# Kernel tuning notes

Hardware: AMD Instinct MI355X
Metric: run time of the kernel (lower is better)

## Reference

```python
import jax, jax.numpy as jnp
import numpy as np

D_MODEL = 4096
NUM_EXPERTS = 64
TOP_K = 2


def setup_inputs() -> dict:
    key = jax.random.key(0)
    kx, kw, kb = jax.random.split(key, 3)
    x = jax.random.normal(kx, (4, 4096, D_MODEL), dtype=jnp.float32)
    # nn.Linear(d_model, num_experts): weight [E, D], bias [E]
    bound = 1.0 / np.sqrt(D_MODEL)
    W = jax.random.uniform(kw, (NUM_EXPERTS, D_MODEL), jnp.float32, -bound, bound)
    b = jax.random.uniform(kb, (NUM_EXPERTS,), jnp.float32, -bound, bound)
    return {"x": x, "W": W, "b": b}


def reference(x, W, b):
    # gate: logits over experts  [B, S, E]
    logits = jnp.einsum("bsd,ed->bse", x, W) + b
    # top-k experts per token
    top_w, top_i = jax.lax.top_k(logits, TOP_K)  # [B, S, K]
    # softmax over the selected k logits
    top_w = jax.nn.softmax(top_w, axis=-1)
    return top_w, top_i
```

## Files before the change

kernel.cpp:

```cpp
#include <hip/hip_runtime.h>
#include <math.h>

#define D_MODEL 4096
#define NE 64
#define TPB 64
#define NSTEPS 64
#define XBUF 16384
#define NXBUF 4
#define WS_SHORTS (256 * 2 * 64 * 8)

typedef __attribute__((ext_vector_type(8))) short short8;
typedef __attribute__((ext_vector_type(16))) float f32x16;

__device__ __forceinline__ void gl_lds(const void* g, void* l) {
    __builtin_amdgcn_global_load_lds(
        (const __attribute__((address_space(1))) unsigned*)g,
        (__attribute__((address_space(3))) unsigned*)l, 16, 0, 0);
}

__device__ __forceinline__ void split8(const float4& a, const float4& c,
                                       short8& h8, short8& l8) {
    union { short8 s; unsigned u[4]; } H, L;
    float vv[8] = {a.x, a.y, a.z, a.w, c.x, c.y, c.z, c.w};
#pragma unroll
    for (int p = 0; p < 4; p++) {
        const float v0 = vv[2*p], v1 = vv[2*p+1];
        const unsigned u0 = __float_as_uint(v0), u1 = __float_as_uint(v1);
        const unsigned r0 = u0 + 0x7fffu + ((u0 >> 16) & 1u);
        const unsigned r1 = u1 + 0x7fffu + ((u1 >> 16) & 1u);
        const float lo0 = v0 - __uint_as_float(r0 & 0xffff0000u);
        const float lo1 = v1 - __uint_as_float(r1 & 0xffff0000u);
        H.u[p] = __builtin_amdgcn_perm(r1, r0, 0x07060302u);
        L.u[p] = __builtin_amdgcn_perm(__float_as_uint(lo1),
                                       __float_as_uint(lo0), 0x07060302u);
    }
    h8 = H.s; l8 = L.s;
}

__global__ void wsplit_kernel(const float* __restrict__ W, short* __restrict__ wsp) {
    const int ck = blockIdx.x, t = threadIdx.x;
    const int nt = t >> 6, l = t & 63;
    const float* wp = W + (size_t)(nt * 32 + (l & 31)) * D_MODEL + ck * 16 + (l >> 5) * 8;
    float4 a = *(const float4*)wp, c = *(const float4*)(wp + 4);
    union { short8 s; unsigned u[4]; } H, L;
    float vv[8] = {a.x, a.y, a.z, a.w, c.x, c.y, c.z, c.w};
#pragma unroll
    for (int p = 0; p < 4; p++) {
        const float v0 = vv[2*p], v1 = vv[2*p+1];
        const unsigned u0 = __float_as_uint(v0), u1 = __float_as_uint(v1);
        const unsigned r0 = u0 + 0x7fffu + ((u0 >> 16) & 1u);
        const unsigned r1 = u1 + 0x7fffu + ((u1 >> 16) & 1u);
        const float lo0 = v0 - __uint_as_float(r0 & 0xffff0000u);
        const float lo1 = v1 - __uint_as_float(r1 & 0xffff0000u);
        const unsigned q0 = __float_as_uint(lo0) + 0x7fffu + ((__float_as_uint(lo0) >> 16) & 1u);
        const unsigned q1 = __float_as_uint(lo1) + 0x7fffu + ((__float_as_uint(lo1) >> 16) & 1u);
        H.u[p] = __builtin_amdgcn_perm(r1, r0, 0x07060302u);
        L.u[p] = __builtin_amdgcn_perm(q1, q0, 0x07060302u);
    }
    const size_t off = ((size_t)(ck * 2 + nt) * 64 + l) * 8;
    *(short8*)(wsp + off)             = H.s;
    *(short8*)(wsp + WS_SHORTS + off) = L.s;
}

#define MF(A_, B_, n_) acc[n_] = __builtin_amdgcn_mfma_f32_32x32x16_bf16( \
                             A_, B_, acc[n_], 0, 0, 0)

__global__ __launch_bounds__(512, 2) void router_pipe(
    const float* __restrict__ x, const short* __restrict__ wsp,
    const float* __restrict__ b, float* __restrict__ out, int T)
{
    __shared__ char smem[NXBUF * XBUF];

    const int tid  = threadIdx.x;
    const int wv   = tid >> 6, lane = tid & 63;
    const int mt   = wv & 1;
    const int kq   = wv >> 1;
    const int tok0 = blockIdx.x * TPB;

    const int tokA = tid >> 4, clA = tid & 15;
    const int tokB = 32 + tokA;
    const float* gx1 = x + (size_t)(tok0 + tokA) * D_MODEL + ((clA ^ (tokA & 15)) * 4);
    const float* gx2 = x + (size_t)(tok0 + tokB) * D_MODEL + ((clA ^ (tokB & 15)) * 4);

#define STAGEX(s_, bi_) do { char* db_ = smem + (bi_) * XBUF + wv * 1024;      \
        gl_lds(gx1 + (size_t)(s_) * 64, db_);                                  \
        gl_lds(gx2 + (size_t)(s_) * 64, db_ + 8192);                           \
        __builtin_amdgcn_sched_barrier(0); } while (0)

#define LDW(s_, W0_, W1_, W2_, W3_) do {                                       \
        const size_t ck_ = (size_t)(s_) * 4 + kq;                              \
        const size_t o0_ = ((ck_ * 2 + 0) * 64 + lane) * 8;                    \
        const size_t o1_ = ((ck_ * 2 + 1) * 64 + lane) * 8;                    \
        W0_ = *(const short8*)(wsp + o0_);                                     \
        W1_ = *(const short8*)(wsp + o1_);                                     \
        W2_ = *(const short8*)(wsp + WS_SHORTS + o0_);                         \
        W3_ = *(const short8*)(wsp + WS_SHORTS + o1_);                         \
        __builtin_amdgcn_sched_barrier(0); } while (0)

#define FENCE(n_) do { asm volatile("s_waitcnt vmcnt(" #n_ ")" ::: "memory");  \
        __builtin_amdgcn_sched_barrier(0); } while (0)
#define BAR do { __builtin_amdgcn_s_barrier();                                 \
        __builtin_amdgcn_sched_barrier(0); } while (0)

    f32x16 acc[2];
#pragma unroll
    for (int e = 0; e < 16; e++) { acc[0][e] = 0.f; acc[1][e] = 0.f; }

    const int row = mt * 32 + (lane & 31);
    const int c0  = kq * 4 + (lane >> 5) * 2;
    const int xo1 = row * 256 + ((c0       ^ (row & 15)) * 16);
    const int xo2 = row * 256 + (((c0 + 1) ^ (row & 15)) * 16);

#define COMPUTE(bi_, W0_, W1_, W2_, W3_) do {                                  \
        const char* buf_ = smem + (bi_) * XBUF;                                \
        float4 xa_ = *(const float4*)(buf_ + xo1);                             \
        float4 xb_ = *(const float4*)(buf_ + xo2);                             \
        short8 Ah_, Al_;                                                       \
        split8(xa_, xb_, Ah_, Al_);                                            \
        MF(Ah_, W0_, 0); MF(Ah_, W2_, 0); MF(Al_, W0_, 0); MF(Al_, W2_, 0);    \
        MF(Ah_, W1_, 1); MF(Ah_, W3_, 1); MF(Al_, W1_, 1); MF(Al_, W3_, 1); } while (0)

    short8 Wa0, Wa1, Wa2, Wa3, Wb0, Wb1, Wb2, Wb3;

    STAGEX(0, 0); STAGEX(1, 1);
    LDW(0, Wa0, Wa1, Wa2, Wa3);

    for (int t = 0; t < NSTEPS - 2; t += 2) {
        LDW(t + 1, Wb0, Wb1, Wb2, Wb3);
        STAGEX(t + 2, (t + 2) & 3);
        FENCE(8); BAR;
        COMPUTE(t & 3, Wa0, Wa1, Wa2, Wa3);
        LDW(t + 2, Wa0, Wa1, Wa2, Wa3);
        STAGEX(t + 3, (t + 3) & 3);
        FENCE(8); BAR;
        COMPUTE((t + 1) & 3, Wb0, Wb1, Wb2, Wb3);
    }
    LDW(NSTEPS - 1, Wb0, Wb1, Wb2, Wb3);
    FENCE(6); BAR;
    COMPUTE((NSTEPS - 2) & 3, Wa0, Wa1, Wa2, Wa3);
    FENCE(0); BAR;
    COMPUTE((NSTEPS - 1) & 3, Wb0, Wb1, Wb2, Wb3);

    __syncthreads();

    float* red = (float*)smem;
    auto store_slab = [&](int slab) {
        float* sl = red + ((size_t)slab * 64 + lane) * 32;
#pragma unroll
        for (int q = 0; q < 8; q++) {
            const int nt = q >> 2, rg = (q & 3) * 4;
            *(float4*)(sl + ((q + lane) & 7) * 4) =
                make_float4(acc[nt][rg], acc[nt][rg+1], acc[nt][rg+2], acc[nt][rg+3]);
        }
    };
    auto add_slab = [&](int slab) {
        const float* sl = red + ((size_t)slab * 64 + lane) * 32;
#pragma unroll
        for (int q = 0; q < 8; q++) {
            const int nt = q >> 2, rg = (q & 3) * 4;
            float4 v = *(const float4*)(sl + ((q + lane) & 7) * 4);
            acc[nt][rg] += v.x; acc[nt][rg+1] += v.y;
            acc[nt][rg+2] += v.z; acc[nt][rg+3] += v.w;
        }
    };
    if (kq >= 2) store_slab(mt * 2 + (kq - 2));
    __syncthreads();
    if (kq < 2) add_slab(mt * 2 + kq);
    __syncthreads();
    if (kq == 1) store_slab(mt);
    __syncthreads();
    if (kq == 0) add_slab(mt);
    __syncthreads();

    float* lg = (float*)(smem + 32768);
    if (kq == 0) {
        const int h = lane >> 5, c31 = lane & 31;
        const float bb0 = b[c31], bb1 = b[32 + c31];
#pragma unroll
        for (int nt = 0; nt < 2; nt++) {
#pragma unroll
            for (int e = 0; e < 16; e++) {
                const int r2 = (e & 3) + 8 * (e >> 2) + 4 * h;
                lg[(mt * 32 + r2) * 68 + nt * 32 + c31] = acc[nt][e] + (nt ? bb1 : bb0);
            }
        }
    }
    __syncthreads();

    if (tid < TPB) {
        const float4* rowp = (const float4*)(lg + tid * 68);
        float v0 = -INFINITY, v1 = -INFINITY;
        int i0 = 0, i1 = 0;
#pragma unroll
        for (int q = 0; q < 16; q++) {
            float4 v4 = rowp[q];
            float vs[4] = {v4.x, v4.y, v4.z, v4.w};
#pragma unroll
            for (int j = 0; j < 4; j++) {
                const int e = q * 4 + j;
                const float v = vs[j];
                if (v > v0)      { v1 = v0; i1 = i0; v0 = v; i0 = e; }
                else if (v > v1) { v1 = v;  i1 = e; }
            }
        }
        const float e1 = expf(v1 - v0);
        const float w0 = 1.f / (1.f + e1);
        const int tok = tok0 + tid;
        out[tok * 2 + 0] = w0;
        out[tok * 2 + 1] = e1 * w0;
        float* oi = out + (size_t)T * 2;
        oi[tok * 2 + 0] = (float)i0;
        oi[tok * 2 + 1] = (float)i1;
    }
}

__global__ __launch_bounds__(512, 4) void router_fb(
    const float* __restrict__ x, const float* __restrict__ W,
    const float* __restrict__ b, float* __restrict__ out, int T)
{
    __shared__ short smem[16384];
    const int tid = threadIdx.x;
    const int wv = tid >> 6, lane = tid & 63;
    const int tok0 = blockIdx.x * 32;
    const int row = lane & 31, kh = lane >> 5;
    const float* gx = x + (size_t)(tok0 + row) * D_MODEL + wv * 512 + kh * 8;
    f32x16 acc[2];
#pragma unroll
    for (int e = 0; e < 16; e++) { acc[0][e] = 0.f; acc[1][e] = 0.f; }
    for (int s = 0; s < 32; s++) {
        const float* g = gx + (size_t)s * 16;
        float4 xa = *(const float4*)g, xb = *(const float4*)(g + 4);
        const int k0 = wv * 512 + s * 16 + kh * 8;
        const float* w0 = W + (size_t)row * D_MODEL + k0;
        const float* w1 = W + (size_t)(32 + row) * D_MODEL + k0;
        short8 Ah, Al, B0h, B0l, B1h, B1l;
        split8(xa, xb, Ah, Al);
        split8(*(const float4*)w0, *(const float4*)(w0 + 4), B0h, B0l);
        split8(*(const float4*)w1, *(const float4*)(w1 + 4), B1h, B1l);
        MF(Ah, B0h, 0); MF(Ah, B0l, 0); MF(Al, B0h, 0); MF(Al, B0l, 0);
        MF(Ah, B1h, 1); MF(Ah, B1l, 1); MF(Al, B1h, 1); MF(Al, B1l, 1);
    }
    float* red = (float*)smem;
    auto store_slab = [&](int slab) {
        float* sl = red + ((size_t)slab * 64 + lane) * 32;
#pragma unroll
        for (int q = 0; q < 8; q++) {
            const int nt = q >> 2, rg = (q & 3) * 4;
            *(float4*)(sl + ((q + lane) & 7) * 4) =
                make_float4(acc[nt][rg], acc[nt][rg+1], acc[nt][rg+2], acc[nt][rg+3]);
        }
    };
    auto add_slab = [&](int slab) {
        const float* sl = red + ((size_t)slab * 64 + lane) * 32;
#pragma unroll
        for (int q = 0; q < 8; q++) {
            const int nt = q >> 2, rg = (q & 3) * 4;
            float4 v = *(const float4*)(sl + ((q + lane) & 7) * 4);
            acc[nt][rg] += v.x; acc[nt][rg+1] += v.y;
            acc[nt][rg+2] += v.z; acc[nt][rg+3] += v.w;
        }
    };
    __syncthreads();
    if (wv >= 4) store_slab(wv - 4);
    __syncthreads();
    if (wv < 4) add_slab(wv);
    __syncthreads();
    if (wv == 2 || wv == 3) store_slab(wv - 2);
    __syncthreads();
    if (wv < 2) add_slab(wv);
    __syncthreads();
    if (wv == 1) store_slab(0);
    __syncthreads();
    if (wv == 0) add_slab(0);
    __syncthreads();
    float* lg = (float*)smem;
    if (wv == 0) {
        const int h = lane >> 5, c31 = lane & 31;
        const float bb0 = b[c31], bb1 = b[32 + c31];
#pragma unroll
        for (int nt = 0; nt < 2; nt++)
#pragma unroll
            for (int e = 0; e < 16; e++) {
                const int r2 = (e & 3) + 8 * (e >> 2) + 4 * h;
                lg[r2 * 68 + nt * 32 + c31] = acc[nt][e] + (nt ? bb1 : bb0);
            }
    }
    __syncthreads();
    if (tid < 32) {
        const float4* rowp = (const float4*)(lg + tid * 68);
        float v0 = -INFINITY, v1 = -INFINITY;
        int i0 = 0, i1 = 0;
#pragma unroll
        for (int q = 0; q < 16; q++) {
            float4 v4 = rowp[q];
            float vs[4] = {v4.x, v4.y, v4.z, v4.w};
#pragma unroll
            for (int j = 0; j < 4; j++) {
                const float v = vs[j];
                if (v > v0)      { v1 = v0; i1 = i0; v0 = v; i0 = q*4+j; }
                else if (v > v1) { v1 = v;  i1 = q*4+j; }
            }
        }
        const float e1 = expf(v1 - v0);
        const float w0 = 1.f / (1.f + e1);
        const int tok = tok0 + tid;
        out[tok * 2 + 0] = w0;
        out[tok * 2 + 1] = e1 * w0;
        float* oi = out + (size_t)T * 2;
        oi[tok * 2 + 0] = (float)i0;
        oi[tok * 2 + 1] = (float)i1;
    }
}

extern "C" void kernel_launch(void* const* d_in, const int* in_sizes, int n_in,
                              void* d_out, int out_size, void* d_ws, size_t ws_size,
                              hipStream_t stream) {
    const float* x = (const float*)d_in[0];
    const float* W = (const float*)d_in[1];
    const float* b = (const float*)d_in[2];
    float* out = (float*)d_out;
    short* wsp = (short*)d_ws;
    const int T = in_sizes[0] / D_MODEL;

    const bool pre = (ws_size >= (size_t)(2 * WS_SHORTS) * sizeof(short));
    if (pre) {
        hipLaunchKernelGGL(wsplit_kernel, dim3(256), dim3(128), 0, stream, W, wsp);
        hipLaunchKernelGGL(router_pipe, dim3(T / TPB), dim3(512), 0, stream,
                           x, wsp, b, out, T);
    } else {
        hipLaunchKernelGGL(router_fb, dim3(T / 32), dim3(512), 0, stream,
                           x, W, b, out, T);
    }
}
```

Before: 67.20 us.

## Restructure x staging into larger double-buffered stages with split W prefetch

Replaces the four-slot, 64-step LDS pipeline with two 64 KB buffers covering 256 columns per stage, cutting the loop to 16 steps. Each wave now issues eight global-to-LDS loads per stage and prefetches W fragments in half-stage groups, so each step runs four MFMA chunks with one barrier instead of one chunk per barrier. The aim is fewer barriers and more memory parallelism per step. The cost is 128 KB of LDS per block, which likely conflicts with __launch_bounds__(512,2) occupancy, plus more live W registers.

```diff
diff --git a/kernel.cpp b/kernel.cpp
--- a/kernel.cpp
+++ b/kernel.cpp
@@ -4,9 +4,8 @@
 #define D_MODEL 4096
 #define NE 64
 #define TPB 64
-#define NSTEPS 64
-#define XBUF 16384
-#define NXBUF 4
+#define NSTEPS 16
+#define XBUF 65536
 #define WS_SHORTS (256 * 2 * 64 * 8)
 
 typedef __attribute__((ext_vector_type(8))) short short8;
@@ -69,7 +68,7 @@
     const float* __restrict__ x, const short* __restrict__ wsp,
     const float* __restrict__ b, float* __restrict__ out, int T)
 {
-    __shared__ char smem[NXBUF * XBUF];
+    __shared__ char smem[2 * XBUF];
 
     const int tid  = threadIdx.x;
     const int wv   = tid >> 6, lane = tid & 63;
@@ -77,24 +76,31 @@
     const int kq   = wv >> 1;
     const int tok0 = blockIdx.x * TPB;
 
-    const int tokA = tid >> 4, clA = tid & 15;
-    const int tokB = 32 + tokA;
-    const float* gx1 = x + (size_t)(tok0 + tokA) * D_MODEL + ((clA ^ (tokA & 15)) * 4);
-    const float* gx2 = x + (size_t)(tok0 + tokB) * D_MODEL + ((clA ^ (tokB & 15)) * 4);
-
-#define STAGEX(s_, bi_) do { char* db_ = smem + (bi_) * XBUF + wv * 1024;      \
-        gl_lds(gx1 + (size_t)(s_) * 64, db_);                                  \
-        gl_lds(gx2 + (size_t)(s_) * 64, db_ + 8192);                           \
+    const int rA  = wv * 4 + (lane >> 4);
+    const int clA = lane & 15;
+    const float* gx0 = x + (size_t)(tok0 + rA) * D_MODEL + ((clA ^ (rA & 15)) * 4);
+    const float* gx1 = gx0 + (size_t)32 * D_MODEL;
+    char* const stb = smem + wv * 8192;
+
+#define STAGEX(s_, bi_) do { char* d_ = stb + (bi_) * XBUF;                    \
+        const float* g0_ = gx0 + (s_) * 256;                                   \
+        const float* g1_ = gx1 + (s_) * 256;                                   \
+        gl_lds(g0_,       d_);        gl_lds(g0_ + 64,  d_ + 1024);            \
+        gl_lds(g0_ + 128, d_ + 2048); gl_lds(g0_ + 192, d_ + 3072);            \
+        gl_lds(g1_,       d_ + 4096); gl_lds(g1_ + 64,  d_ + 5120);            \
+        gl_lds(g1_ + 128, d_ + 6144); gl_lds(g1_ + 192, d_ + 7168);            \
         __builtin_amdgcn_sched_barrier(0); } while (0)
 
-#define LDW(s_, W0_, W1_, W2_, W3_) do {                                       \
-        const size_t ck_ = (size_t)(s_) * 4 + kq;                              \
-        const size_t o0_ = ((ck_ * 2 + 0) * 64 + lane) * 8;                    \
-        const size_t o1_ = ((ck_ * 2 + 1) * 64 + lane) * 8;                    \
-        W0_ = *(const short8*)(wsp + o0_);                                     \
-        W1_ = *(const short8*)(wsp + o1_);                                     \
-        W2_ = *(const short8*)(wsp + WS_SHORTS + o0_);                         \
-        W3_ = *(const short8*)(wsp + WS_SHORTS + o1_);                         \
+#define LDW1(cg_, Wh0_, Wh1_, Wl0_, Wl1_) do {                                 \
+        const size_t o0_ = (((size_t)(cg_) * 2 + 0) * 64 + lane) * 8;          \
+        const size_t o1_ = (((size_t)(cg_) * 2 + 1) * 64 + lane) * 8;          \
+        Wh0_ = *(const short8*)(wsp + o0_);                                    \
+        Wh1_ = *(const short8*)(wsp + o1_);                                    \
+        Wl0_ = *(const short8*)(wsp + WS_SHORTS + o0_);                        \
+        Wl1_ = *(const short8*)(wsp + WS_SHORTS + o1_);                        \
+    } while (0)
+#define LDWH(cg_, P) do { LDW1((cg_), P##0h0, P##0h1, P##0l0, P##0l1);         \
+        LDW1((cg_) + 1, P##1h0, P##1h1, P##1l0, P##1l1);                       \
         __builtin_amdgcn_sched_barrier(0); } while (0)
 
 #define FENCE(n_) do { asm volatile("s_waitcnt vmcnt(" #n_ ")" ::: "memory");  \
@@ -106,40 +112,56 @@
 #pragma unroll
     for (int e = 0; e < 16; e++) { acc[0][e] = 0.f; acc[1][e] = 0.f; }
 
-    const int row = mt * 32 + (lane & 31);
-    const int c0  = kq * 4 + (lane >> 5) * 2;
-    const int xo1 = row * 256 + ((c0       ^ (row & 15)) * 16);
-    const int xo2 = row * 256 + (((c0 + 1) ^ (row & 15)) * 16);
-
-#define COMPUTE(bi_, W0_, W1_, W2_, W3_) do {                                  \
-        const char* buf_ = smem + (bi_) * XBUF;                                \
-        float4 xa_ = *(const float4*)(buf_ + xo1);                             \
-        float4 xb_ = *(const float4*)(buf_ + xo2);                             \
-        short8 Ah_, Al_;                                                       \
-        split8(xa_, xb_, Ah_, Al_);                                            \
-        MF(Ah_, W0_, 0); MF(Ah_, W2_, 0); MF(Al_, W0_, 0); MF(Al_, W2_, 0);    \
-        MF(Ah_, W1_, 1); MF(Ah_, W3_, 1); MF(Al_, W1_, 1); MF(Al_, W3_, 1); } while (0)
-
-    short8 Wa0, Wa1, Wa2, Wa3, Wb0, Wb1, Wb2, Wb3;
-
-    STAGEX(0, 0); STAGEX(1, 1);
-    LDW(0, Wa0, Wa1, Wa2, Wa3);
-
-    for (int t = 0; t < NSTEPS - 2; t += 2) {
-        LDW(t + 1, Wb0, Wb1, Wb2, Wb3);
-        STAGEX(t + 2, (t + 2) & 3);
-        FENCE(8); BAR;
-        COMPUTE(t & 3, Wa0, Wa1, Wa2, Wa3);
-        LDW(t + 2, Wa0, Wa1, Wa2, Wa3);
-        STAGEX(t + 3, (t + 3) & 3);
-        FENCE(8); BAR;
-        COMPUTE((t + 1) & 3, Wb0, Wb1, Wb2, Wb3);
-    }
-    LDW(NSTEPS - 1, Wb0, Wb1, Wb2, Wb3);
-    FENCE(6); BAR;
-    COMPUTE((NSTEPS - 2) & 3, Wa0, Wa1, Wa2, Wa3);
-    FENCE(0); BAR;
-    COMPUTE((NSTEPS - 1) & 3, Wb0, Wb1, Wb2, Wb3);
+    const int rw = lane & 31, khalf = lane >> 5;
+    const int blane = (rw >> 2) * 8192 + (mt * 4 + kq) * 1024 + (rw & 3) * 256;
+    const int swz = rw & 15;
+#define XOFF(ch_, j_) ((((4 * (ch_) + 2 * khalf + (j_)) ^ swz)) * 16)
+    const int o00 = XOFF(0, 0), o01 = XOFF(0, 1);
+    const int o10 = XOFF(1, 0), o11 = XOFF(1, 1);
+    const int o20 = XOFF(2, 0), o21 = XOFF(2, 1);
+    const int o30 = XOFF(3, 0), o31 = XOFF(3, 1);
+
+#define CCHUNK(bp_, oA_, oB_, Wh0_, Wh1_, Wl0_, Wl1_) do {                     \
+        float4 xa_ = *(const float4*)((bp_) + oA_);                            \
+        float4 xb_ = *(const float4*)((bp_) + oB_);                            \
+        short8 Ah_, Al_; split8(xa_, xb_, Ah_, Al_);                           \
+        MF(Ah_, Wh0_, 0); MF(Ah_, Wl0_, 0); MF(Al_, Wh0_, 0); MF(Al_, Wl0_, 0);\
+        MF(Ah_, Wh1_, 1); MF(Ah_, Wl1_, 1); MF(Al_, Wh1_, 1); MF(Al_, Wl1_, 1);\
+    } while (0)
+
+#define COMPA(bi_) do { const char* bp_ = smem + (bi_) * XBUF + blane;         \
+        CCHUNK(bp_, o00, o01, A0h0, A0h1, A0l0, A0l1);                         \
+        CCHUNK(bp_, o10, o11, A1h0, A1h1, A1l0, A1l1); } while (0)
+#define COMPB(bi_) do { const char* bp_ = smem + (bi_) * XBUF + blane;         \
+        CCHUNK(bp_, o20, o21, B0h0, B0h1, B0l0, B0l1);                         \
+        CCHUNK(bp_, o30, o31, B1h0, B1h1, B1l0, B1l1); } while (0)
+
+    short8 A0h0, A0h1, A0l0, A0l1, A1h0, A1h1, A1l0, A1l1;
+    short8 B0h0, B0h1, B0l0, B0l1, B1h0, B1h1, B1l0, B1l1;
+
+    STAGEX(0, 0);
+    LDWH(0 * 16 + kq * 4, A);
+
+    for (int s = 0; s < NSTEPS - 1; ++s) {
+        const int cg = s * 16 + kq * 4;
+        LDWH(cg + 2, B);
+        FENCE(8);
+        BAR;
+        STAGEX(s + 1, (s + 1) & 1);
+        COMPA(s & 1);
+        LDWH(cg + 16, A);
+        FENCE(16);
+        COMPB(s & 1);
+    }
+    {
+        const int s = NSTEPS - 1;
+        LDWH(s * 16 + kq * 4 + 2, B);
+        FENCE(8);
+        BAR;
+        COMPA(s & 1);
+        FENCE(0);
+        COMPB(s & 1);
+    }
 
     __syncthreads();
 
```

New measurement: 64.82 us. 1.04x faster.
